# Performance work log

Measured on AMD Instinct MI355X. Metric: run time of the kernel, lower is better.

## Reference

```python
import jax, jax.numpy as jnp
import numpy as np

L, D, H, V, B, S = 12, 768, 12, 50257, 1, 2048
F = 4 * D
HD = D // H
EPS = 1e-5
NEG = -1e38


def setup_inputs() -> dict:
    key = jax.random.key(0)
    ks = jax.random.split(key, 12)
    s = 0.02
    f32 = jnp.float32
    return {
        "x": jax.random.normal(ks[0], (B, S, D), f32),
        "ln1_g": jnp.ones((L, D), f32), "ln1_b": jnp.zeros((L, D), f32),
        "Wq": jax.random.normal(ks[1], (L, D, D), f32) * s,
        "Wk": jax.random.normal(ks[2], (L, D, D), f32) * s,
        "Wv": jax.random.normal(ks[3], (L, D, D), f32) * s,
        "Wo": jax.random.normal(ks[4], (L, D, D), f32) * s,
        "bo": jnp.zeros((L, D), f32),
        "ln2_g": jnp.ones((L, D), f32), "ln2_b": jnp.zeros((L, D), f32),
        "Wfc": jax.random.normal(ks[5], (L, D, F), f32) * s,
        "bfc": jnp.zeros((L, F), f32),
        "Wp": jax.random.normal(ks[6], (L, F, D), f32) * s,
        "bp": jnp.zeros((L, D), f32),
        "lnf_g": jnp.ones((D,), f32), "lnf_b": jnp.zeros((D,), f32),
        "Wlm": jax.random.normal(ks[7], (D, V), f32) * s,
    }


def _ln(h, g, b):
    mu = h.mean(-1, keepdims=True)
    var = ((h - mu) ** 2).mean(-1, keepdims=True)
    return (h - mu) * jax.lax.rsqrt(var + EPS) * g + b


def reference(x, ln1_g, ln1_b, Wq, Wk, Wv, Wo, bo, ln2_g, ln2_b,
              Wfc, bfc, Wp, bp, lnf_g, lnf_b, Wlm):
    Bx, Sx, Dx = x.shape
    # additive causal mask, NOTE: original has no 1/sqrt(head_dim) scaling
    mask = (1.0 - jnp.tril(jnp.ones((Sx, Sx), x.dtype))) * NEG

    def block(h, p):
        g1, b1, wq, wk, wv, wo, bo_, g2, b2, wfc, bfc_, wp, bp_ = p
        hn = _ln(h, g1, b1)
        def heads(w):  # [B,S,D] -> [B,H,S,hd]
            return (hn @ w).reshape(Bx, Sx, H, HD).transpose(0, 2, 1, 3)
        q, k, v = heads(wq), heads(wk), heads(wv)
        scores = jnp.einsum('bhqd,bhkd->bhqk', q, k) + mask
        probs = jax.nn.softmax(scores, axis=-1)
        attn = jnp.einsum('bhqk,bhkd->bhqd', probs, v)
        attn = attn.transpose(0, 2, 1, 3).reshape(Bx, Sx, Dx)
        h = h + attn @ wo + bo_
        hn2 = _ln(h, g2, b2)
        ff = jax.nn.gelu(hn2 @ wfc + bfc_, approximate=False) @ wp + bp_
        return h + ff, None

    h, _ = jax.lax.scan(
        block, x,
        (ln1_g, ln1_b, Wq, Wk, Wv, Wo, bo, ln2_g, ln2_b, Wfc, bfc, Wp, bp))
    return _ln(h, lnf_g, lnf_b) @ Wlm
```

## Files before the change

kernel.cpp:

```cpp
#include <hip/hip_runtime.h>
#include <hip/hip_bf16.h>
#include <math.h>

typedef unsigned short ushort;
typedef __attribute__((ext_vector_type(8))) short short8;
typedef __attribute__((ext_vector_type(4))) short short4v;
typedef __attribute__((ext_vector_type(4))) float f4v;

constexpr int SEQ = 2048;
constexpr int DM  = 768;
constexpr int NH  = 12;
constexpr int HDM = 64;
constexpr int FF  = 3072;
constexpr int NL  = 12;
constexpr int NV  = 50257;
constexpr int NVP = 50304;

__device__ inline ushort f2bf(float f) {
    union { float f; unsigned u; } v; v.f = f;
    unsigned r = v.u + 0x7fffu + ((v.u >> 16) & 1u);
    return (ushort)(r >> 16);
}

__device__ __forceinline__ void gld16(const ushort* g, ushort* l) {
    __builtin_amdgcn_global_load_lds(
        (const __attribute__((address_space(1))) void*)g,
        (__attribute__((address_space(3))) void*)l, 16, 0, 0);
}

__global__ __launch_bounds__(256) void ln_kernel(const float* __restrict__ x,
                                                 const float* __restrict__ g,
                                                 const float* __restrict__ b,
                                                 ushort* __restrict__ out) {
    int row = blockIdx.x;
    int t = threadIdx.x;
    const float* xr = x + (size_t)row * DM;
    float v0 = xr[t], v1 = xr[t + 256], v2 = xr[t + 512];
    float s = v0 + v1 + v2;
    float s2 = v0 * v0 + v1 * v1 + v2 * v2;
    for (int m = 1; m < 64; m <<= 1) { s += __shfl_xor(s, m); s2 += __shfl_xor(s2, m); }
    __shared__ float ls[4], ls2[4];
    int w = t >> 6;
    if ((t & 63) == 0) { ls[w] = s; ls2[w] = s2; }
    __syncthreads();
    s = ls[0] + ls[1] + ls[2] + ls[3];
    s2 = ls2[0] + ls2[1] + ls2[2] + ls2[3];
    float mu = s * (1.0f / DM);
    float var = s2 * (1.0f / DM) - mu * mu;
    float rs = rsqrtf(var + 1e-5f);
    ushort* o = out + (size_t)row * DM;
    o[t]       = f2bf((v0 - mu) * rs * g[t]       + b[t]);
    o[t + 256] = f2bf((v1 - mu) * rs * g[t + 256] + b[t + 256]);
    o[t + 512] = f2bf((v2 - mu) * rs * g[t + 512] + b[t + 512]);
}

__global__ __launch_bounds__(256) void cvt_t(const float* __restrict__ in, size_t inL,
                                             ushort* __restrict__ out, size_t outL,
                                             int K, int N) {
    __shared__ ushort T[64][72];
    int l = blockIdx.z;
    const float* ip = in + (size_t)l * inL;
    ushort* op = out + (size_t)l * outL;
    int kb = blockIdx.x * 64, nb = blockIdx.y * 64;
    int t = threadIdx.x;
    int nl = t & 63, ks = (t >> 6) * 16;
    int n = nb + nl;
    #pragma unroll
    for (int j = 0; j < 16; ++j) {
        float f = (n < N) ? ip[(size_t)(kb + ks + j) * N + n] : 0.f;
        T[nl][ks + j] = f2bf(f);
    }
    __syncthreads();
    int r = t >> 2, c4 = (t & 3) * 16;
    *(short8*)(op + (size_t)(nb + r) * K + kb + c4)     = *(const short8*)&T[r][c4];
    *(short8*)(op + (size_t)(nb + r) * K + kb + c4 + 8) = *(const short8*)&T[r][c4 + 8];
}

template <int BM, int BN, int EPI>
__global__ __launch_bounds__(256) void gemmT(const ushort* __restrict__ A,
                                             const ushort* __restrict__ Bt,
                                             const float* __restrict__ bias,
                                             const float* __restrict__ res,
                                             void* __restrict__ outp,
                                             ushort* __restrict__ vt,
                                             int M, int N, int K, int ldOut) {
    constexpr int FM = BM / 32;
    constexpr int FN = BN / 32;
    __shared__ ushort As[BM * 64];
    __shared__ ushort Bs[BN * 64];
    int tid = threadIdx.x, lane = tid & 63, wave = tid >> 6;
    int wm = (wave >> 1) * (BM / 2), wn = (wave & 1) * (BN / 2);
    int mBase = blockIdx.x * BM, nBase = blockIdx.y * BN;
    int lr = lane & 15, lg = lane >> 4;
    int swz = (lr & 7) << 3;

    f4v acc[FM][FN];
    #pragma unroll
    for (int i = 0; i < FM; ++i)
        #pragma unroll
        for (int j = 0; j < FN; ++j) acc[i][j] = (f4v){0.f, 0.f, 0.f, 0.f};

    int cBase = wave * 64 + lane;

    for (int kb = 0; kb < K; kb += 64) {
        #pragma unroll
        for (int i = 0; i < BM / 32; ++i) {
            int c = i * 256 + cBase;
            int row = c >> 3;
            int kc = (c & 7) ^ (row & 7);
            gld16(A + (size_t)(mBase + row) * K + kb + kc * 8,
                  As + (size_t)(i * 256 + wave * 64) * 8);
        }
        #pragma unroll
        for (int i = 0; i < BN / 32; ++i) {
            int c = i * 256 + cBase;
            int row = c >> 3;
            int kc = (c & 7) ^ (row & 7);
            gld16(Bt + (size_t)(nBase + row) * K + kb + kc * 8,
                  Bs + (size_t)(i * 256 + wave * 64) * 8);
        }
        __syncthreads();
        #pragma unroll
        for (int kk = 0; kk < 2; ++kk) {
            short8 a[FM], b[FN];
            #pragma unroll
            for (int fr = 0; fr < FM; ++fr)
                a[fr] = *(const short8*)(As + (wm + fr * 16 + lr) * 64 + ((((kk * 4 + lg) << 3)) ^ swz));
            #pragma unroll
            for (int fc = 0; fc < FN; ++fc)
                b[fc] = *(const short8*)(Bs + (wn + fc * 16 + lr) * 64 + ((((kk * 4 + lg) << 3)) ^ swz));
            #pragma unroll
            for (int fr = 0; fr < FM; ++fr)
                #pragma unroll
                for (int fc = 0; fc < FN; ++fc)
                    acc[fr][fc] = __builtin_amdgcn_mfma_f32_16x16x32_bf16(a[fr], b[fc], acc[fr][fc], 0, 0, 0);
        }
        __syncthreads();
    }

    if constexpr (EPI == 4) {
        if (nBase < 1536) {
            #pragma unroll
            for (int fr = 0; fr < FM; ++fr)
                #pragma unroll
                for (int fc = 0; fc < FN; ++fc)
                    #pragma unroll
                    for (int r = 0; r < 4; ++r) {
                        int row = mBase + wm + fr * 16 + 4 * lg + r;
                        int col = nBase + wn + fc * 16 + lr;
                        ((ushort*)outp)[(size_t)row * ldOut + col] = f2bf(acc[fr][fc][r]);
                    }
        } else {
            #pragma unroll
            for (int fr = 0; fr < FM; ++fr)
                #pragma unroll
                for (int fc = 0; fc < FN; ++fc) {
                    short4v pk;
                    #pragma unroll
                    for (int r = 0; r < 4; ++r) pk[r] = (short)f2bf(acc[fr][fc][r]);
                    int d  = nBase - 1536 + wn + fc * 16 + lr;
                    int m0 = mBase + wm + fr * 16 + 4 * lg;
                    *(short4v*)(vt + (size_t)d * SEQ + m0) = pk;
                }
        }
        return;
    }

    #pragma unroll
    for (int fr = 0; fr < FM; ++fr)
        #pragma unroll
        for (int fc = 0; fc < FN; ++fc)
            #pragma unroll
            for (int r = 0; r < 4; ++r) {
                int row = mBase + wm + fr * 16 + 4 * lg + r;
                int col = nBase + wn + fc * 16 + lr;
                float v = acc[fr][fc][r];
                if constexpr (EPI == 0) {
                    ((ushort*)outp)[(size_t)row * ldOut + col] = f2bf(v);
                } else if constexpr (EPI == 1) {
                    v += bias[col] + res[(size_t)row * ldOut + col];
                    ((float*)outp)[(size_t)row * ldOut + col] = v;
                } else if constexpr (EPI == 2) {
                    v += bias[col];
                    v = 0.5f * v * (1.f + erff(v * 0.70710678118f));
                    ((ushort*)outp)[(size_t)row * ldOut + col] = f2bf(v);
                } else {
                    if (col < N) ((float*)outp)[(size_t)row * ldOut + col] = v;
                }
            }
}

__global__ __launch_bounds__(256) void attn_v5(const ushort* __restrict__ Qg,
                                               const ushort* __restrict__ Kg,
                                               const ushort* __restrict__ Vt,
                                               ushort* __restrict__ Og) {
    __shared__ ushort Ks[64 * 64];
    __shared__ ushort Vs[64 * 64];
    __shared__ ushort Ps[4 * 16 * 64];
    int tid = threadIdx.x, lane = tid & 63, wave = tid >> 6;
    int flat = blockIdx.x;
    int qb   = (SEQ / 64) - 1 - (flat / NH);
    int head = flat % NH;
    int lr = lane & 15, lg = lane >> 4;
    int qr0 = qb * 64 + wave * 16;
    int hoff = head * HDM;
    int swz = (lr & 7) << 3;

    short8 qf0 = *(const short8*)(Qg + (size_t)(qr0 + lr) * 2304 + hoff + lg * 8);
    short8 qf1 = *(const short8*)(Qg + (size_t)(qr0 + lr) * 2304 + hoff + 32 + lg * 8);

    const f4v fz = {0.f, 0.f, 0.f, 0.f};
    f4v o[4];
    o[0] = fz; o[1] = fz; o[2] = fz; o[3] = fz;
    float mrow[4] = {-1e30f, -1e30f, -1e30f, -1e30f};
    float lsum[4] = {0.f, 0.f, 0.f, 0.f};

    int c0 = wave * 64 + lane;
    int c1 = c0 + 256;
    int r0 = c0 >> 3, kc0 = ((c0 & 7) ^ (r0 & 7)) * 8;
    int r1 = c1 >> 3, kc1 = ((c1 & 7) ^ (r1 & 7)) * 8;

    for (int kb = 0; kb <= qb; ++kb) {
        gld16(Kg + (size_t)(kb * 64 + r0) * 2304 + hoff + kc0, Ks + (size_t)(wave * 64) * 8);
        gld16(Kg + (size_t)(kb * 64 + r1) * 2304 + hoff + kc1, Ks + (size_t)(256 + wave * 64) * 8);
        gld16(Vt + (size_t)(hoff + r0) * SEQ + kb * 64 + kc0,  Vs + (size_t)(wave * 64) * 8);
        gld16(Vt + (size_t)(hoff + r1) * SEQ + kb * 64 + kc1,  Vs + (size_t)(256 + wave * 64) * 8);
        __syncthreads();

        f4v s[4];
        #pragma unroll
        for (int n = 0; n < 4; ++n) {
            const ushort* kr = Ks + (n * 16 + lr) * 64;
            short8 k0 = *(const short8*)(kr + ((lg << 3) ^ swz));
            short8 k1 = *(const short8*)(kr + ((((4 + lg) << 3)) ^ swz));
            f4v z = fz;
            z = __builtin_amdgcn_mfma_f32_16x16x32_bf16(qf0, k0, z, 0, 0, 0);
            s[n] = __builtin_amdgcn_mfma_f32_16x16x32_bf16(qf1, k1, z, 0, 0, 0);
        }
        if (kb == qb) {
            #pragma unroll
            for (int n = 0; n < 4; ++n)
                #pragma unroll
                for (int r = 0; r < 4; ++r) {
                    int col = kb * 64 + n * 16 + lr;
                    int row = qr0 + 4 * lg + r;
                    if (col > row) s[n][r] = -1e38f;
                }
        }

        int sub = lr & 7, hi = lr >> 3;
        #pragma unroll
        for (int r = 0; r < 4; ++r) {
            float mx = fmaxf(fmaxf(s[0][r], s[1][r]), fmaxf(s[2][r], s[3][r]));
            mx = fmaxf(mx, __shfl_xor(mx, 1));
            mx = fmaxf(mx, __shfl_xor(mx, 2));
            mx = fmaxf(mx, __shfl_xor(mx, 4));
            mx = fmaxf(mx, __shfl_xor(mx, 8));
            float mnew = fmaxf(mrow[r], mx);
            float corr = __expf(mrow[r] - mnew);
            float ps0 = __expf(s[0][r] - mnew);
            float ps1 = __expf(s[1][r] - mnew);
            float ps2 = __expf(s[2][r] - mnew);
            float ps3 = __expf(s[3][r] - mnew);
            float rs = ps0 + ps1 + ps2 + ps3;
            rs += __shfl_xor(rs, 1);
            rs += __shfl_xor(rs, 2);
            rs += __shfl_xor(rs, 4);
            rs += __shfl_xor(rs, 8);
            lsum[r] = lsum[r] * corr + rs;
            mrow[r] = mnew;
            o[0][r] *= corr; o[1][r] *= corr; o[2][r] *= corr; o[3][r] *= corr;
            int prow = 4 * lg + r;
            ushort* pb = Ps + wave * 1024 + prow * 64;
            int px = prow & 7;
            pb[(((0 + hi) ^ px) << 3) | sub] = f2bf(ps0);
            pb[(((2 + hi) ^ px) << 3) | sub] = f2bf(ps1);
            pb[(((4 + hi) ^ px) << 3) | sub] = f2bf(ps2);
            pb[(((6 + hi) ^ px) << 3) | sub] = f2bf(ps3);
        }
        __syncthreads();

        #pragma unroll
        for (int kk = 0; kk < 2; ++kk) {
            short8 pa = *(const short8*)(Ps + wave * 1024 + lr * 64 + ((((kk * 4 + lg) << 3)) ^ swz));
            #pragma unroll
            for (int dn = 0; dn < 4; ++dn) {
                short8 vb = *(const short8*)(Vs + (dn * 16 + lr) * 64 + ((((kk * 4 + lg) << 3)) ^ swz));
                o[dn] = __builtin_amdgcn_mfma_f32_16x16x32_bf16(pa, vb, o[dn], 0, 0, 0);
            }
        }
        __syncthreads();
    }

    #pragma unroll
    for (int dn = 0; dn < 4; ++dn)
        #pragma unroll
        for (int r = 0; r < 4; ++r) {
            int row = qr0 + 4 * lg + r;
            Og[(size_t)row * DM + hoff + dn * 16 + lr] = f2bf(o[dn][r] / lsum[r]);
        }
}

template <int EPI>
__global__ __launch_bounds__(256) void gemm64(const ushort* __restrict__ A,
                                              const float* __restrict__ B,
                                              const float* __restrict__ bias,
                                              const float* __restrict__ res,
                                              void* __restrict__ outp,
                                              int M, int N, int K) {
    __shared__ ushort As[64][64];
    __shared__ ushort Bs[64][72];
    int tid = threadIdx.x;
    int lane = tid & 63, wave = tid >> 6;
    int wm = (wave >> 1) * 32, wn = (wave & 1) * 32;
    int mBase = blockIdx.x * 64, nBase = blockIdx.y * 64;
    int lr = lane & 15, lg = lane >> 4;

    const f4v fz = {0.f, 0.f, 0.f, 0.f};
    f4v acc[2][2];
    acc[0][0] = fz; acc[0][1] = fz; acc[1][0] = fz; acc[1][1] = fz;

    int ar = tid >> 2, ac = (tid & 3) * 16;
    int br = tid >> 2, bc = (tid & 3) * 16;

    for (int kb = 0; kb < K; kb += 64) {
        const short8* ag = (const short8*)(A + (size_t)(mBase + ar) * K + kb + ac);
        *(short8*)&As[ar][ac]     = ag[0];
        *(short8*)&As[ar][ac + 8] = ag[1];
        if constexpr (EPI == 3) {
            #pragma unroll
            for (int j = 0; j < 16; ++j) {
                int col = nBase + bc + j;
                float f = (col < N) ? B[(size_t)(kb + br) * N + col] : 0.f;
                Bs[bc + j][br] = f2bf(f);
            }
        } else {
            const float4* bg = (const float4*)(B + (size_t)(kb + br) * N + nBase + bc);
            float fv[16];
            *(float4*)&fv[0]  = bg[0];
            *(float4*)&fv[4]  = bg[1];
            *(float4*)&fv[8]  = bg[2];
            *(float4*)&fv[12] = bg[3];
            #pragma unroll
            for (int j = 0; j < 16; ++j) Bs[bc + j][br] = f2bf(fv[j]);
        }
        __syncthreads();
        #pragma unroll
        for (int kk = 0; kk < 2; ++kk) {
            short8 a0 = *(const short8*)&As[wm + lr][kk * 32 + lg * 8];
            short8 a1 = *(const short8*)&As[wm + 16 + lr][kk * 32 + lg * 8];
            short8 b0 = *(const short8*)&Bs[wn + lr][kk * 32 + lg * 8];
            short8 b1 = *(const short8*)&Bs[wn + 16 + lr][kk * 32 + lg * 8];
            acc[0][0] = __builtin_amdgcn_mfma_f32_16x16x32_bf16(a0, b0, acc[0][0], 0, 0, 0);
            acc[0][1] = __builtin_amdgcn_mfma_f32_16x16x32_bf16(a0, b1, acc[0][1], 0, 0, 0);
            acc[1][0] = __builtin_amdgcn_mfma_f32_16x16x32_bf16(a1, b0, acc[1][0], 0, 0, 0);
            acc[1][1] = __builtin_amdgcn_mfma_f32_16x16x32_bf16(a1, b1, acc[1][1], 0, 0, 0);
        }
        __syncthreads();
    }

    #pragma unroll
    for (int fm = 0; fm < 2; ++fm)
        #pragma unroll
        for (int fn = 0; fn < 2; ++fn)
            #pragma unroll
            for (int r = 0; r < 4; ++r) {
                int row = mBase + wm + fm * 16 + 4 * lg + r;
                int col = nBase + wn + fn * 16 + lr;
                float v = acc[fm][fn][r];
                if constexpr (EPI == 0) {
                    ((ushort*)outp)[(size_t)row * N + col] = f2bf(v);
                } else if constexpr (EPI == 1) {
                    v += bias[col] + res[(size_t)row * N + col];
                    ((float*)outp)[(size_t)row * N + col] = v;
                } else if constexpr (EPI == 2) {
                    v += bias[col];
                    v = 0.5f * v * (1.f + erff(v * 0.70710678118f));
                    ((ushort*)outp)[(size_t)row * N + col] = f2bf(v);
                } else {
                    if (col < N) ((float*)outp)[(size_t)row * N + col] = v;
                }
            }
}

__global__ __launch_bounds__(256) void attn_stage(const ushort* __restrict__ Qg,
                                                  const ushort* __restrict__ Kg,
                                                  const ushort* __restrict__ Vg,
                                                  ushort* __restrict__ Og,
                                                  int ld) {
    __shared__ ushort Ks[64][64];
    __shared__ ushort Vs[64][72];
    __shared__ ushort Ps[4][16][64];
    int tid = threadIdx.x, lane = tid & 63, wave = tid >> 6;
    int qb = blockIdx.x, head = blockIdx.y;
    int lr = lane & 15, lg = lane >> 4;
    int qr0 = qb * 64 + wave * 16;
    size_t hoff = (size_t)head * HDM;

    short8 qf0 = *(const short8*)(Qg + (size_t)(qr0 + lr) * ld + hoff + lg * 8);
    short8 qf1 = *(const short8*)(Qg + (size_t)(qr0 + lr) * ld + hoff + 32 + lg * 8);

    const f4v fz = {0.f, 0.f, 0.f, 0.f};
    f4v o[4];
    o[0] = fz; o[1] = fz; o[2] = fz; o[3] = fz;
    float mrow[4] = {-1e30f, -1e30f, -1e30f, -1e30f};
    float lsum[4] = {0.f, 0.f, 0.f, 0.f};

    int r_ = tid >> 2, c_ = (tid & 3) * 16;

    for (int kb = 0; kb <= qb; ++kb) {
        const short8* kg = (const short8*)(Kg + (size_t)(kb * 64 + r_) * ld + hoff + c_);
        *(short8*)&Ks[r_][c_]     = kg[0];
        *(short8*)&Ks[r_][c_ + 8] = kg[1];
        const short8* vg = (const short8*)(Vg + (size_t)(kb * 64 + r_) * ld + hoff + c_);
        short8 v0 = vg[0], v1 = vg[1];
        #pragma unroll
        for (int j = 0; j < 8; ++j) {
            Vs[c_ + j][r_]     = (ushort)v0[j];
            Vs[c_ + 8 + j][r_] = (ushort)v1[j];
        }
        __syncthreads();

        f4v s[4];
        #pragma unroll
        for (int n = 0; n < 4; ++n) {
            short8 k0 = *(const short8*)&Ks[n * 16 + lr][lg * 8];
            short8 k1 = *(const short8*)&Ks[n * 16 + lr][32 + lg * 8];
            f4v z = fz;
            z = __builtin_amdgcn_mfma_f32_16x16x32_bf16(qf0, k0, z, 0, 0, 0);
            s[n] = __builtin_amdgcn_mfma_f32_16x16x32_bf16(qf1, k1, z, 0, 0, 0);
        }
        if (kb == qb) {
            #pragma unroll
            for (int n = 0; n < 4; ++n)
                #pragma unroll
                for (int r = 0; r < 4; ++r) {
                    int col = kb * 64 + n * 16 + lr;
                    int row = qr0 + 4 * lg + r;
                    if (col > row) s[n][r] = -1e38f;
                }
        }

        #pragma unroll
        for (int r = 0; r < 4; ++r) {
            float mx = fmaxf(fmaxf(s[0][r], s[1][r]), fmaxf(s[2][r], s[3][r]));
            mx = fmaxf(mx, __shfl_xor(mx, 1));
            mx = fmaxf(mx, __shfl_xor(mx, 2));
            mx = fmaxf(mx, __shfl_xor(mx, 4));
            mx = fmaxf(mx, __shfl_xor(mx, 8));
            float mnew = fmaxf(mrow[r], mx);
            float corr = __expf(mrow[r] - mnew);
            float ps0 = __expf(s[0][r] - mnew);
            float ps1 = __expf(s[1][r] - mnew);
            float ps2 = __expf(s[2][r] - mnew);
            float ps3 = __expf(s[3][r] - mnew);
            float rs = ps0 + ps1 + ps2 + ps3;
            rs += __shfl_xor(rs, 1);
            rs += __shfl_xor(rs, 2);
            rs += __shfl_xor(rs, 4);
            rs += __shfl_xor(rs, 8);
            lsum[r] = lsum[r] * corr + rs;
            mrow[r] = mnew;
            o[0][r] *= corr; o[1][r] *= corr; o[2][r] *= corr; o[3][r] *= corr;
            Ps[wave][4 * lg + r][0 * 16 + lr] = f2bf(ps0);
            Ps[wave][4 * lg + r][1 * 16 + lr] = f2bf(ps1);
            Ps[wave][4 * lg + r][2 * 16 + lr] = f2bf(ps2);
            Ps[wave][4 * lg + r][3 * 16 + lr] = f2bf(ps3);
        }
        __syncthreads();

        #pragma unroll
        for (int kk = 0; kk < 2; ++kk) {
            short8 pa = *(const short8*)&Ps[wave][lr][kk * 32 + lg * 8];
            #pragma unroll
            for (int dn = 0; dn < 4; ++dn) {
                short8 vb = *(const short8*)&Vs[dn * 16 + lr][kk * 32 + lg * 8];
                o[dn] = __builtin_amdgcn_mfma_f32_16x16x32_bf16(pa, vb, o[dn], 0, 0, 0);
            }
        }
        __syncthreads();
    }

    #pragma unroll
    for (int dn = 0; dn < 4; ++dn)
        #pragma unroll
        for (int r = 0; r < 4; ++r) {
            int row = qr0 + 4 * lg + r;
            Og[(size_t)row * DM + hoff + dn * 16 + lr] = f2bf(o[dn][r] / lsum[r]);
        }
}

extern "C" void kernel_launch(void* const* d_in, const int* in_sizes, int n_in,
                              void* d_out, int out_size, void* d_ws, size_t ws_size,
                              hipStream_t stream) {
    const float* x     = (const float*)d_in[0];
    const float* ln1_g = (const float*)d_in[1];
    const float* ln1_b = (const float*)d_in[2];
    const float* Wq    = (const float*)d_in[3];
    const float* Wk    = (const float*)d_in[4];
    const float* Wv    = (const float*)d_in[5];
    const float* Wo    = (const float*)d_in[6];
    const float* bo    = (const float*)d_in[7];
    const float* ln2_g = (const float*)d_in[8];
    const float* ln2_b = (const float*)d_in[9];
    const float* Wfc   = (const float*)d_in[10];
    const float* bfc   = (const float*)d_in[11];
    const float* Wp    = (const float*)d_in[12];
    const float* bp    = (const float*)d_in[13];
    const float* lnf_g = (const float*)d_in[14];
    const float* lnf_b = (const float*)d_in[15];
    const float* Wlm   = (const float*)d_in[16];

    dim3 blk(256);

    size_t offs[12];
    size_t need = 0;
    size_t sizes[11] = {
        (size_t)SEQ * DM * 4,
        (size_t)SEQ * DM * 2,
        (size_t)SEQ * 2304 * 2,
        (size_t)SEQ * DM * 2,
        (size_t)SEQ * FF * 2,
        (size_t)DM * SEQ * 2,
        (size_t)NL * 2304 * DM * 2,
        (size_t)NL * DM * DM * 2,
        (size_t)NL * FF * DM * 2,
        (size_t)NL * DM * FF * 2,
        (size_t)NVP * DM * 2,
    };
    for (int i = 0; i < 11; ++i) { offs[i] = need; need += sizes[i]; }
    offs[11] = need;

    if (ws_size >= need) {
        char* ws = (char*)d_ws;
        float*  h    = (float*)(ws + offs[0]);
        ushort* hn   = (ushort*)(ws + offs[1]);
        ushort* qkv  = (ushort*)(ws + offs[2]);
        ushort* ab_  = (ushort*)(ws + offs[3]);
        ushort* fb_  = (ushort*)(ws + offs[4]);
        ushort* vt   = (ushort*)(ws + offs[5]);
        ushort* qkvw = (ushort*)(ws + offs[6]);
        ushort* wow  = (ushort*)(ws + offs[7]);
        ushort* fcw  = (ushort*)(ws + offs[8]);
        ushort* wpw  = (ushort*)(ws + offs[9]);
        ushort* lmw  = (ushort*)(ws + offs[10]);

        hipMemcpyAsync(h, x, (size_t)SEQ * DM * 4, hipMemcpyDeviceToDevice, stream);

        cvt_t<<<dim3(12, 12, NL), blk, 0, stream>>>(Wq, (size_t)DM * DM, qkvw,               (size_t)2304 * DM, DM, DM);
        cvt_t<<<dim3(12, 12, NL), blk, 0, stream>>>(Wk, (size_t)DM * DM, qkvw + DM * DM,     (size_t)2304 * DM, DM, DM);
        cvt_t<<<dim3(12, 12, NL), blk, 0, stream>>>(Wv, (size_t)DM * DM, qkvw + 2 * DM * DM, (size_t)2304 * DM, DM, DM);
        cvt_t<<<dim3(12, 12, NL), blk, 0, stream>>>(Wo, (size_t)DM * DM, wow, (size_t)DM * DM, DM, DM);
        cvt_t<<<dim3(12, 48, NL), blk, 0, stream>>>(Wfc, (size_t)DM * FF, fcw, (size_t)FF * DM, DM, FF);
        cvt_t<<<dim3(48, 12, NL), blk, 0, stream>>>(Wp,  (size_t)FF * DM, wpw, (size_t)DM * FF, FF, DM);
        cvt_t<<<dim3(12, 786, 1), blk, 0, stream>>>(Wlm, 0, lmw, 0, DM, NV);

        for (int l = 0; l < NL; ++l) {
            const ushort* qw = qkvw + (size_t)l * 2304 * DM;
            ln_kernel<<<SEQ, blk, 0, stream>>>(h, ln1_g + l * DM, ln1_b + l * DM, hn);
            gemmT<128, 128, 4><<<dim3(16, 18), blk, 0, stream>>>(hn, qw, nullptr, nullptr, qkv, vt, SEQ, 2304, DM, 2304);
            attn_v5<<<dim3((SEQ / 64) * NH), blk, 0, stream>>>(qkv, qkv + 768, vt, ab_);
            gemmT<128, 64, 1><<<dim3(16, 12), blk, 0, stream>>>(ab_, wow + (size_t)l * DM * DM, bo + l * DM, h, h, nullptr, SEQ, DM, DM, DM);
            ln_kernel<<<SEQ, blk, 0, stream>>>(h, ln2_g + l * DM, ln2_b + l * DM, hn);
            gemmT<128, 128, 2><<<dim3(16, 24), blk, 0, stream>>>(hn, fcw + (size_t)l * FF * DM, bfc + l * FF, nullptr, fb_, nullptr, SEQ, FF, DM, FF);
            gemmT<128, 64, 1><<<dim3(16, 12), blk, 0, stream>>>(fb_, wpw + (size_t)l * DM * FF, bp + l * DM, h, h, nullptr, SEQ, DM, FF, DM);
        }
        ln_kernel<<<SEQ, blk, 0, stream>>>(h, lnf_g, lnf_b, hn);
        gemmT<128, 128, 3><<<dim3(16, NVP / 128), blk, 0, stream>>>(hn, lmw, nullptr, nullptr, d_out, nullptr, SEQ, NV, DM, NV);
        return;
    }

    char* ws = (char*)d_ws;
    float*  h   = (float*)ws;   ws += (size_t)SEQ * DM * 4;
    ushort* hn  = (ushort*)ws;  ws += (size_t)SEQ * DM * 2;
    ushort* qb_ = (ushort*)ws;  ws += (size_t)SEQ * DM * 2;
    ushort* kb_ = (ushort*)ws;  ws += (size_t)SEQ * DM * 2;
    ushort* vb_ = (ushort*)ws;  ws += (size_t)SEQ * DM * 2;
    ushort* ab_ = (ushort*)ws;  ws += (size_t)SEQ * DM * 2;
    ushort* fb_ = (ushort*)ws;  ws += (size_t)SEQ * FF * 2;

    hipMemcpyAsync(h, x, (size_t)SEQ * DM * 4, hipMemcpyDeviceToDevice, stream);

    dim3 gdd(SEQ / 64, DM / 64);
    dim3 gdf(SEQ / 64, FF / 64);
    dim3 gda(SEQ / 64, NH);
    dim3 gdl(SEQ / 64, (NV + 63) / 64);

    for (int l = 0; l < NL; ++l) {
        ln_kernel<<<SEQ, blk, 0, stream>>>(h, ln1_g + l * DM, ln1_b + l * DM, hn);
        gemm64<0><<<gdd, blk, 0, stream>>>(hn, Wq + (size_t)l * DM * DM, nullptr, nullptr, qb_, SEQ, DM, DM);
        gemm64<0><<<gdd, blk, 0, stream>>>(hn, Wk + (size_t)l * DM * DM, nullptr, nullptr, kb_, SEQ, DM, DM);
        gemm64<0><<<gdd, blk, 0, stream>>>(hn, Wv + (size_t)l * DM * DM, nullptr, nullptr, vb_, SEQ, DM, DM);
        attn_stage<<<gda, blk, 0, stream>>>(qb_, kb_, vb_, ab_, DM);
        gemm64<1><<<gdd, blk, 0, stream>>>(ab_, Wo + (size_t)l * DM * DM, bo + l * DM, h, h, SEQ, DM, DM);
        ln_kernel<<<SEQ, blk, 0, stream>>>(h, ln2_g + l * DM, ln2_b + l * DM, hn);
        gemm64<2><<<gdf, blk, 0, stream>>>(hn, Wfc + (size_t)l * DM * FF, bfc + l * FF, nullptr, fb_, SEQ, FF, DM);
        gemm64<1><<<gdd, blk, 0, stream>>>(fb_, Wp + (size_t)l * FF * DM, bp + l * DM, h, h, SEQ, DM, FF);
    }
    ln_kernel<<<SEQ, blk, 0, stream>>>(h, lnf_g, lnf_b, hn);
    gemm64<3><<<gdl, blk, 0, stream>>>(hn, Wlm, nullptr, nullptr, d_out, SEQ, NV, DM);
}
```

Baseline: 2.700 ms.

## Double-buffer LDS tiles in GEMM and attention kernels

```diff
diff --git a/kernel.cpp b/kernel.cpp
--- a/kernel.cpp
+++ b/kernel.cpp
@@ -76,7 +76,7 @@
     *(short8*)(op + (size_t)(nb + r) * K + kb + c4 + 8) = *(const short8*)&T[r][c4 + 8];
 }
 
-template <int BM, int BN, int EPI>
+template <int BM, int BN, int EPI, bool DB>
 __global__ __launch_bounds__(256) void gemmT(const ushort* __restrict__ A,
                                              const ushort* __restrict__ Bt,
                                              const float* __restrict__ bias,
@@ -86,8 +86,11 @@
                                              int M, int N, int K, int ldOut) {
     constexpr int FM = BM / 32;
     constexpr int FN = BN / 32;
-    __shared__ ushort As[BM * 64];
-    __shared__ ushort Bs[BN * 64];
+    constexpr int NBUF = DB ? 2 : 1;
+    constexpr int ASZ = BM * 64;
+    constexpr int BSZ = BN * 64;
+    __shared__ ushort As[NBUF * ASZ];
+    __shared__ ushort Bs[NBUF * BSZ];
     int tid = threadIdx.x, lane = tid & 63, wave = tid >> 6;
     int wm = (wave >> 1) * (BM / 2), wn = (wave & 1) * (BN / 2);
     int mBase = blockIdx.x * BM, nBase = blockIdx.y * BN;
@@ -102,14 +105,14 @@
 
     int cBase = wave * 64 + lane;
 
-    for (int kb = 0; kb < K; kb += 64) {
+    auto stage = [&](int kb, int buf) {
         #pragma unroll
         for (int i = 0; i < BM / 32; ++i) {
             int c = i * 256 + cBase;
             int row = c >> 3;
             int kc = (c & 7) ^ (row & 7);
             gld16(A + (size_t)(mBase + row) * K + kb + kc * 8,
-                  As + (size_t)(i * 256 + wave * 64) * 8);
+                  As + buf * ASZ + (size_t)(i * 256 + wave * 64) * 8);
         }
         #pragma unroll
         for (int i = 0; i < BN / 32; ++i) {
@@ -117,25 +120,44 @@
             int row = c >> 3;
             int kc = (c & 7) ^ (row & 7);
             gld16(Bt + (size_t)(nBase + row) * K + kb + kc * 8,
-                  Bs + (size_t)(i * 256 + wave * 64) * 8);
-        }
-        __syncthreads();
+                  Bs + buf * BSZ + (size_t)(i * 256 + wave * 64) * 8);
+        }
+    };
+    auto compute = [&](int buf) {
         #pragma unroll
         for (int kk = 0; kk < 2; ++kk) {
             short8 a[FM], b[FN];
             #pragma unroll
             for (int fr = 0; fr < FM; ++fr)
-                a[fr] = *(const short8*)(As + (wm + fr * 16 + lr) * 64 + ((((kk * 4 + lg) << 3)) ^ swz));
+                a[fr] = *(const short8*)(As + buf * ASZ + (wm + fr * 16 + lr) * 64 + ((((kk * 4 + lg) << 3)) ^ swz));
             #pragma unroll
             for (int fc = 0; fc < FN; ++fc)
-                b[fc] = *(const short8*)(Bs + (wn + fc * 16 + lr) * 64 + ((((kk * 4 + lg) << 3)) ^ swz));
+                b[fc] = *(const short8*)(Bs + buf * BSZ + (wn + fc * 16 + lr) * 64 + ((((kk * 4 + lg) << 3)) ^ swz));
             #pragma unroll
             for (int fr = 0; fr < FM; ++fr)
                 #pragma unroll
                 for (int fc = 0; fc < FN; ++fc)
                     acc[fr][fc] = __builtin_amdgcn_mfma_f32_16x16x32_bf16(a[fr], b[fc], acc[fr][fc], 0, 0, 0);
         }
-        __syncthreads();
+    };
+
+    if constexpr (DB) {
+        stage(0, 0);
+        __syncthreads();
+        int cur = 0;
+        for (int kb = 0; kb < K; kb += 64) {
+            if (kb + 64 < K) stage(kb + 64, cur ^ 1);
+            compute(cur);
+            __syncthreads();
+            cur ^= 1;
+        }
+    } else {
+        for (int kb = 0; kb < K; kb += 64) {
+            stage(kb, 0);
+            __syncthreads();
+            compute(0);
+            __syncthreads();
+        }
     }
 
     if constexpr (EPI == 4) {
@@ -190,12 +212,12 @@
             }
 }
 
-__global__ __launch_bounds__(256) void attn_v5(const ushort* __restrict__ Qg,
+__global__ __launch_bounds__(256) void attn_v6(const ushort* __restrict__ Qg,
                                                const ushort* __restrict__ Kg,
                                                const ushort* __restrict__ Vt,
                                                ushort* __restrict__ Og) {
-    __shared__ ushort Ks[64 * 64];
-    __shared__ ushort Vs[64 * 64];
+    __shared__ ushort Ks[2 * 4096];
+    __shared__ ushort Vs[2 * 4096];
     __shared__ ushort Ps[4 * 16 * 64];
     int tid = threadIdx.x, lane = tid & 63, wave = tid >> 6;
     int flat = blockIdx.x;
@@ -220,17 +242,24 @@
     int r0 = c0 >> 3, kc0 = ((c0 & 7) ^ (r0 & 7)) * 8;
     int r1 = c1 >> 3, kc1 = ((c1 & 7) ^ (r1 & 7)) * 8;
 
+    auto stageKV = [&](int kb, int buf) {
+        gld16(Kg + (size_t)(kb * 64 + r0) * 2304 + hoff + kc0, Ks + buf * 4096 + wave * 512);
+        gld16(Kg + (size_t)(kb * 64 + r1) * 2304 + hoff + kc1, Ks + buf * 4096 + 2048 + wave * 512);
+        gld16(Vt + (size_t)(hoff + r0) * SEQ + kb * 64 + kc0,  Vs + buf * 4096 + wave * 512);
+        gld16(Vt + (size_t)(hoff + r1) * SEQ + kb * 64 + kc1,  Vs + buf * 4096 + 2048 + wave * 512);
+    };
+
+    stageKV(0, 0);
+    __syncthreads();
+    int cur = 0;
+
     for (int kb = 0; kb <= qb; ++kb) {
-        gld16(Kg + (size_t)(kb * 64 + r0) * 2304 + hoff + kc0, Ks + (size_t)(wave * 64) * 8);
-        gld16(Kg + (size_t)(kb * 64 + r1) * 2304 + hoff + kc1, Ks + (size_t)(256 + wave * 64) * 8);
-        gld16(Vt + (size_t)(hoff + r0) * SEQ + kb * 64 + kc0,  Vs + (size_t)(wave * 64) * 8);
-        gld16(Vt + (size_t)(hoff + r1) * SEQ + kb * 64 + kc1,  Vs + (size_t)(256 + wave * 64) * 8);
-        __syncthreads();
+        if (kb < qb) stageKV(kb + 1, cur ^ 1);
 
         f4v s[4];
         #pragma unroll
         for (int n = 0; n < 4; ++n) {
-            const ushort* kr = Ks + (n * 16 + lr) * 64;
+            const ushort* kr = Ks + cur * 4096 + (n * 16 + lr) * 64;
             short8 k0 = *(const short8*)(kr + ((lg << 3) ^ swz));
             short8 k1 = *(const short8*)(kr + ((((4 + lg) << 3)) ^ swz));
             f4v z = fz;
@@ -285,11 +314,12 @@
             short8 pa = *(const short8*)(Ps + wave * 1024 + lr * 64 + ((((kk * 4 + lg) << 3)) ^ swz));
             #pragma unroll
             for (int dn = 0; dn < 4; ++dn) {
-                short8 vb = *(const short8*)(Vs + (dn * 16 + lr) * 64 + ((((kk * 4 + lg) << 3)) ^ swz));
+                short8 vb = *(const short8*)(Vs + cur * 4096 + (dn * 16 + lr) * 64 + ((((kk * 4 + lg) << 3)) ^ swz));
                 o[dn] = __builtin_amdgcn_mfma_f32_16x16x32_bf16(pa, vb, o[dn], 0, 0, 0);
             }
         }
         __syncthreads();
+        cur ^= 1;
     }
 
     #pragma unroll
@@ -558,15 +588,15 @@
         for (int l = 0; l < NL; ++l) {
             const ushort* qw = qkvw + (size_t)l * 2304 * DM;
             ln_kernel<<<SEQ, blk, 0, stream>>>(h, ln1_g + l * DM, ln1_b + l * DM, hn);
-            gemmT<128, 128, 4><<<dim3(16, 18), blk, 0, stream>>>(hn, qw, nullptr, nullptr, qkv, vt, SEQ, 2304, DM, 2304);
-            attn_v5<<<dim3((SEQ / 64) * NH), blk, 0, stream>>>(qkv, qkv + 768, vt, ab_);
-            gemmT<128, 64, 1><<<dim3(16, 12), blk, 0, stream>>>(ab_, wow + (size_t)l * DM * DM, bo + l * DM, h, h, nullptr, SEQ, DM, DM, DM);
+            gemmT<128, 128, 4, true><<<dim3(16, 18), blk, 0, stream>>>(hn, qw, nullptr, nullptr, qkv, vt, SEQ, 2304, DM, 2304);
+            attn_v6<<<dim3((SEQ / 64) * NH), blk, 0, stream>>>(qkv, qkv + 768, vt, ab_);
+            gemmT<128, 64, 1, true><<<dim3(16, 12), blk, 0, stream>>>(ab_, wow + (size_t)l * DM * DM, bo + l * DM, h, h, nullptr, SEQ, DM, DM, DM);
             ln_kernel<<<SEQ, blk, 0, stream>>>(h, ln2_g + l * DM, ln2_b + l * DM, hn);
-            gemmT<128, 128, 2><<<dim3(16, 24), blk, 0, stream>>>(hn, fcw + (size_t)l * FF * DM, bfc + l * FF, nullptr, fb_, nullptr, SEQ, FF, DM, FF);
-            gemmT<128, 64, 1><<<dim3(16, 12), blk, 0, stream>>>(fb_, wpw + (size_t)l * DM * FF, bp + l * DM, h, h, nullptr, SEQ, DM, FF, DM);
+            gemmT<128, 128, 2, true><<<dim3(16, 24), blk, 0, stream>>>(hn, fcw + (size_t)l * FF * DM, bfc + l * FF, nullptr, fb_, nullptr, SEQ, FF, DM, FF);
+            gemmT<128, 64, 1, true><<<dim3(16, 12), blk, 0, stream>>>(fb_, wpw + (size_t)l * DM * FF, bp + l * DM, h, h, nullptr, SEQ, DM, FF, DM);
         }
         ln_kernel<<<SEQ, blk, 0, stream>>>(h, lnf_g, lnf_b, hn);
-        gemmT<128, 128, 3><<<dim3(16, NVP / 128), blk, 0, stream>>>(hn, lmw, nullptr, nullptr, d_out, nullptr, SEQ, NV, DM, NV);
+        gemmT<128, 128, 3, false><<<dim3(16, NVP / 128), blk, 0, stream>>>(hn, lmw, nullptr, nullptr, d_out, nullptr, SEQ, NV, DM, NV);
         return;
     }
 
```

After: 2.648 ms. No clear change (-1.9%).
